# Optimization experiments

Hardware: AMD Instinct MI355X
Metric: run time of the kernel (lower is better)

The kernel has to match this reference:

```python
import jax, jax.numpy as jnp
import numpy as np

# config constants (match init_kwargs)
C = 1024
NH = 16
HS = C // NH
CHUNK = 64          # attn_chunk_size
TOPK = 32           # attn_topk
WINDOW = 4096       # kv_cache_window_size
MIN_KV = 16384      # min_kv_cache_size
MAX_KV = 32768      # max_kv_cache_size
SHORT = 4096        # short_sequence_criteria
CT = 65536          # incoming kv-cache length


def setup_inputs() -> dict:
    key = jax.random.key(0)
    ks = jax.random.split(key, 7)
    s = 1.0 / np.sqrt(C)
    return {
        "x": jax.random.normal(ks[0], (C,), jnp.float32),
        "k_cache": jax.random.normal(ks[1], (1, CT, C), jnp.float32),
        "v_cache": jax.random.normal(ks[2], (1, CT, C), jnp.float32),
        "Wr": jax.random.normal(ks[3], (C, C), jnp.float32) * s,
        "Wk": jax.random.normal(ks[4], (C, C), jnp.float32) * s,
        "Wv": jax.random.normal(ks[5], (C, C), jnp.float32) * s,
        "Wo": jax.random.normal(ks[6], (C, C), jnp.float32) * s,
    }


def _split_heads(t):  # (1, T, C) -> (1, NH, T, HS)
    return t.reshape(1, t.shape[1], NH, HS).transpose(0, 2, 1, 3)


def _update_kv_cache(q, k_cache, v_cache):
    # q: (1,1,C); caches: (1,CT,C). CT > MIN_KV so compression runs.
    past = CT - WINDOW
    kp = _split_heads(k_cache[:, :past])          # (1,NH,past,HS)
    vp = _split_heads(v_cache[:, :past])
    qh = _split_heads(q)                          # (1,NH,1,HS)
    scores = jnp.einsum("bhqd,bhkd->bhqk", qh, kp) / np.sqrt(HS)
    w = jax.nn.softmax(scores, axis=-1)           # (1,NH,1,past)
    vote = w.sum(axis=-2)                         # (1,NH,past)
    keep = MIN_KV - WINDOW                        # per-head tokens kept
    _, idx = jax.lax.top_k(vote, keep)            # (1,NH,keep), descending vote order
    kpc = jnp.take_along_axis(kp, idx[..., None], axis=2)  # (1,NH,keep,HS)
    vpc = jnp.take_along_axis(vp, idx[..., None], axis=2)
    kpc = kpc.transpose(0, 2, 1, 3).reshape(1, keep, C)
    vpc = vpc.transpose(0, 2, 1, 3).reshape(1, keep, C)
    k_new = jnp.concatenate([kpc, k_cache[:, past:]], axis=1)  # (1, MIN_KV, C)
    v_new = jnp.concatenate([vpc, v_cache[:, past:]], axis=1)
    return k_new, v_new


def reference(x, k_cache, v_cache, Wr, Wk, Wv, Wo):
    x2 = x[None, None, :]                         # (1,1,C)
    q = x2 @ Wr.T
    k = x2 @ Wk.T
    v = x2 @ Wv.T

    # CT > MAX_KV -> compress cache (eviction via attention vote per head)
    k_cache, v_cache = _update_kv_cache(q, k_cache, v_cache)
    CT2 = k_cache.shape[1]                        # MIN_KV = 16384 > SHORT -> sparse path

    num_chunks = CT2 // CHUNK
    kc = k_cache.reshape(1, num_chunks, CHUNK, C)
    vc = v_cache.reshape(1, num_chunks, CHUNK, C)
    chunk_key = kc.mean(axis=2)                   # (1,num_chunks,C)
    chunk_score = jnp.einsum("bqc,bkc->bqk", q, chunk_key)
    _, tidx = jax.lax.top_k(chunk_score[0, 0], TOPK)  # (TOPK,)
    topk_k = kc[:, tidx].reshape(1, TOPK * CHUNK, C)
    topk_v = vc[:, tidx].reshape(1, TOPK * CHUNK, C)

    k_comb = jnp.concatenate([topk_k, k], axis=1)  # (1, TOPK*CHUNK+1, C)
    v_comb = jnp.concatenate([topk_v, v], axis=1)

    qh = _split_heads(q)                          # (1,NH,1,HS)
    kh = _split_heads(k_comb)
    vh = _split_heads(v_comb)
    attn = jax.nn.softmax(
        jnp.einsum("bhqd,bhkd->bhqk", qh, kh) / np.sqrt(HS), axis=-1)
    y = jnp.einsum("bhqk,bhkd->bhqd", attn, vh)   # (1,NH,1,HS)
    y = y.transpose(0, 2, 1, 3).reshape(C)
    y = y @ Wo.T
    return y
```

## Files before the change

kernel.cpp:

```cpp
#include <hip/hip_runtime.h>
#include <stdint.h>

#define C      1024
#define NH     16
#define HS     64
#define CT     65536
#define PAST   61440
#define KEEP   12288
#define NCOMP  192
#define NSEL   32
#define NB     8192
#define NBLK   256
#define FLAGW  8

typedef unsigned long long ull;

#define LD_A(p)   __hip_atomic_load((p), __ATOMIC_RELAXED, __HIP_MEMORY_SCOPE_AGENT)
#define ST_A(p,v) __hip_atomic_store((p), (v), __ATOMIC_RELAXED, __HIP_MEMORY_SCOPE_AGENT)

__device__ __forceinline__ unsigned int desc_key(float f) {
    unsigned int b = __float_as_uint(f);
    return (b >> 31) ? b : (~b & 0x7FFFFFFFu);
}
__device__ __forceinline__ float u_to_f(unsigned int u) {
    unsigned int b = (u & 0x80000000u) ? u : (0x7FFFFFFFu - u);
    return __uint_as_float(b);
}
__device__ __forceinline__ int bin_of(float s, float hi, float scale) {
    int b = (int)((hi - s) * scale);
    return b < 0 ? 0 : (b > NB - 1 ? NB - 1 : b);
}
__device__ __forceinline__ void load_params(const unsigned* umin, const unsigned* umax,
                                            int h, float* hi, float* sc) {
    float h2 = u_to_f(umin[h]);
    float lo = u_to_f(umax[h]);
    float r = h2 - lo;
    *hi = h2;
    *sc = (r > 0.f) ? (float)(NB - 1) / r : 0.f;
}

__device__ __forceinline__ void arrive(unsigned* flag, unsigned ph) {
    __syncthreads();
    if (threadIdx.x == 0) {
        asm volatile("s_waitcnt vmcnt(0)" ::: "memory");
        ST_A(&flag[blockIdx.x * FLAGW], ph);
    }
}
__device__ __forceinline__ void wait_head(unsigned* flag, unsigned ph, int h) {
    if (threadIdx.x < 16)
        while (LD_A(&flag[(h * 16 + threadIdx.x) * FLAGW]) < ph)
            __builtin_amdgcn_s_sleep(2);
    __syncthreads();
}
__device__ __forceinline__ void wait_all(unsigned* flag, unsigned ph) {
    if (threadIdx.x < 256)
        while (LD_A(&flag[threadIdx.x * FLAGW]) < ph)
            __builtin_amdgcn_s_sleep(2);
    __syncthreads();
}

__global__ void k_proj(const float* __restrict__ x, const float* __restrict__ Wr,
                       const float* __restrict__ Wk, const float* __restrict__ Wv,
                       float* __restrict__ q, float* __restrict__ kn, float* __restrict__ vn,
                       unsigned* __restrict__ hc, unsigned* __restrict__ umin,
                       unsigned* __restrict__ umax, ull* __restrict__ cs_fix,
                       unsigned* __restrict__ flag) {
    int gid = blockIdx.x * 256 + threadIdx.x;
    for (int i = gid; i < 2 * NH * NB; i += 196608) hc[i] = 0;
    if (blockIdx.x >= 512 && blockIdx.x < 520)
        flag[(blockIdx.x - 512) * 256 + threadIdx.x] = 0u;
    if (blockIdx.x == 700) {
        if (threadIdx.x < 16) umin[threadIdx.x] = 0xFFFFFFFFu;
        else if (threadIdx.x < 32) umax[threadIdx.x - 16] = 0u;
    }
    if (blockIdx.x == 701 && threadIdx.x < 256) cs_fix[threadIdx.x] = 0ull;

    int w = blockIdx.x * (blockDim.x >> 6) + (threadIdx.x >> 6);
    int lane = threadIdx.x & 63;
    int mat = w >> 10, row = w & 1023;
    const float* W = (mat == 0) ? Wr : (mat == 1) ? Wk : Wv;
    const float4* Wrow = (const float4*)(W + (size_t)row * C);
    const float4* x4 = (const float4*)x;
    float acc = 0.f;
#pragma unroll
    for (int i = 0; i < 4; ++i) {
        float4 a = Wrow[i * 64 + lane];
        float4 b = x4[i * 64 + lane];
        acc += a.x * b.x + a.y * b.y + a.z * b.z + a.w * b.w;
    }
#pragma unroll
    for (int off = 32; off; off >>= 1) acc += __shfl_xor(acc, off);
    if (lane == 0) { (mat == 0 ? q : (mat == 1 ? kn : vn))[row] = acc; }
}

__global__ __launch_bounds__(1024, 2) void k_mega(
        const float* __restrict__ kc, const float* __restrict__ s_dummy,
        const float* __restrict__ vc,
        unsigned* __restrict__ umin, unsigned* __restrict__ umax,
        unsigned* __restrict__ hist, unsigned* __restrict__ cnt,
        ull* __restrict__ G, unsigned* __restrict__ stok,
        ull* __restrict__ cs_fix, float* __restrict__ part,
        const float* __restrict__ q, const float* __restrict__ kn,
        const float* __restrict__ vn, const float* __restrict__ Wo,
        float* __restrict__ yg, float* __restrict__ out,
        float* __restrict__ s, unsigned* __restrict__ flag) {
    const int bid = blockIdx.x, tid = threadIdx.x;
    const int lane = tid & 63, wave = tid >> 6;
    const int h = bid >> 4, seg = bid & 15;
    __shared__ __align__(16) char smem[49664];
    __shared__ unsigned shT, shN;
    __shared__ unsigned wsum[16];
    __shared__ long long wredl[16];

    {
        float (*scl)[16][17] = (float(*)[16][17])smem;
        float* smn = (float*)(smem + 18496);
        float* smx = (float*)(smem + 19520);
        const int t0 = bid * 256 + wave * 16;
        const float4* q4 = (const float4*)q;
        float4 qv[4];
#pragma unroll
        for (int i = 0; i < 4; ++i) qv[i] = q4[i * 64 + lane];
        float mnv[4] = {3.4e38f, 3.4e38f, 3.4e38f, 3.4e38f};
        float mxv[4] = {-3.4e38f, -3.4e38f, -3.4e38f, -3.4e38f};
        for (int tt = 0; tt < 16; ++tt) {
            const float4* row = (const float4*)(kc + (size_t)(t0 + tt) * C);
            float acc[4];
#pragma unroll
            for (int i = 0; i < 4; ++i) {
                float4 a = row[i * 64 + lane];
                acc[i] = a.x * qv[i].x + a.y * qv[i].y + a.z * qv[i].z + a.w * qv[i].w;
            }
#pragma unroll
            for (int off = 8; off; off >>= 1) {
#pragma unroll
                for (int i = 0; i < 4; ++i) acc[i] += __shfl_xor(acc[i], off);
            }
            if ((lane & 15) == 0) {
                int g = lane >> 4;
#pragma unroll
                for (int i = 0; i < 4; ++i) {
                    scl[wave][4 * i + g][tt] = acc[i];
                    mnv[i] = fminf(mnv[i], acc[i]);
                    mxv[i] = fmaxf(mxv[i], acc[i]);
                }
            }
        }
        __syncthreads();
        int tt2 = lane & 15;
#pragma unroll
        for (int r = 0; r < 4; ++r) {
            int h2 = r * 4 + (lane >> 4);
            ST_A(&s[(size_t)h2 * CT + t0 + tt2], scl[wave][h2][tt2]);
        }
        if (bid < 240) {
            if ((lane & 15) == 0) {
                int g = lane >> 4;
#pragma unroll
                for (int i = 0; i < 4; ++i) {
                    smn[wave * 16 + 4 * i + g] = mnv[i];
                    smx[wave * 16 + 4 * i + g] = mxv[i];
                }
            }
            __syncthreads();
            if (tid < 16) {
                float mn = smn[tid], mx = smx[tid];
                for (int w2 = 1; w2 < 16; ++w2) {
                    mn = fminf(mn, smn[w2 * 16 + tid]);
                    mx = fmaxf(mx, smx[w2 * 16 + tid]);
                }
                atomicMin(&umin[tid], desc_key(mx));
                atomicMax(&umax[tid], desc_key(mn));
            }
        } else {
            int k = tid >> 8, sub = tid & 255, hh = sub >> 4, tt = sub & 15;
            long long f = 0;
#pragma unroll
            for (int w2 = 0; w2 < 4; ++w2)
                f += llrintf(scl[4 * k + w2][hh][tt] * 16777216.f);
#pragma unroll
            for (int off = 32; off; off >>= 1) f += __shfl_xor(f, off);
            if ((tid & 63) == 0) wredl[wave] = f;
            __syncthreads();
            if ((tid & 255) == 0)
                ST_A(&cs_fix[NCOMP + (bid - 240) * 4 + k],
                     (ull)(wredl[4 * k] + wredl[4 * k + 1] + wredl[4 * k + 2] + wredl[4 * k + 3]));
        }
    }
    arrive(flag, 1); wait_all(flag, 1);

    float hi, sc; load_params(umin, umax, h, &hi, &sc);
    unsigned* lh = (unsigned*)smem;
    float* s_local = (float*)(smem + 32768);

    {
        for (int i = tid; i < NB; i += 1024) lh[i] = 0;
        __syncthreads();
        const float* sh = s + (size_t)h * CT + seg * 3840;
        for (int i = tid; i < 3840; i += 1024) {
            float v = sh[i];
            s_local[i] = v;
            atomicAdd(&lh[bin_of(v, hi, sc)], 1u);
        }
        __syncthreads();
        unsigned* gh = hist + h * NB;
        for (int i = tid; i < NB; i += 1024) {
            unsigned c = lh[i];
            if (c) atomicAdd(&gh[i], c);
        }
    }
    arrive(flag, 2); wait_head(flag, 2, h);

    {
        const unsigned* gh = hist + h * NB;
        unsigned c8[8]; unsigned loc = 0; int b0 = tid * 8;
#pragma unroll
        for (int k = 0; k < 8; ++k) { c8[k] = gh[b0 + k]; loc += c8[k]; }
        unsigned run = loc;
#pragma unroll
        for (int off = 1; off < 64; off <<= 1) {
            unsigned n = __shfl_up(run, off);
            if (lane >= off) run += n;
        }
        if (lane == 63) wsum[wave] = run;
        __syncthreads();
        if (wave == 0 && lane < 16) {
            unsigned v = wsum[lane];
#pragma unroll
            for (int off = 1; off < 16; off <<= 1) {
                unsigned n = __shfl_up(v, off);
                if (lane >= off) v += n;
            }
            wsum[lane] = v;
        }
        __syncthreads();
        unsigned r = run - loc + (wave ? wsum[wave - 1] : 0u);
#pragma unroll
        for (int k = 0; k < 8; ++k) {
            unsigned c = c8[k];
            lh[b0 + k] = r;
            unsigned inc = r + c;
            if (r < KEEP && inc >= KEEP) { shT = (unsigned)(b0 + k); shN = inc; }
            r = inc;
        }
    }
    __syncthreads();
    const unsigned T = shT, ncand = shN;

    {
        unsigned* ch = cnt + h * NB;
        ull* Gh = G + (size_t)h * 65536;
        for (int i = tid; i < 3840; i += 1024) {
            float v = s_local[i];
            int b = bin_of(v, hi, sc);
            if ((unsigned)b <= T) {
                unsigned pos = lh[b] + atomicAdd(&ch[b], 1u);
                ST_A(&Gh[pos], ((ull)desc_key(v) << 16) | (unsigned)(seg * 3840 + i));
            }
        }
    }
    arrive(flag, 3); wait_head(flag, 3, h);

    {
        ull* csl = (ull*)(smem + 48128);
        if (tid < NCOMP) csl[tid] = 0ull;
        __syncthreads();
        const ull* Gh = G + (size_t)h * 65536;
        for (unsigned p = seg * 1024 + tid; p < ncand; p += 16384) {
            ull pk = Gh[p];
            unsigned u = (unsigned)(pk >> 16);
            float v = u_to_f(u);
            int b = bin_of(v, hi, sc);
            unsigned start = lh[b];
            unsigned end = (b == NB - 1) ? ncand : lh[b + 1];
            unsigned rank = start;
            for (unsigned j = start; j < end; ++j) rank += (Gh[j] < pk) ? 1u : 0u;
            if (rank < KEEP) {
                ST_A(&stok[h * KEEP + rank], (unsigned)(pk & 0xFFFFull));
                long long f = llrintf(v * 16777216.f);
                atomicAdd(&csl[rank >> 6], (ull)f);
            }
        }
        __syncthreads();
        if (tid < NCOMP) {
            ull c = csl[tid];
            if (c) atomicAdd(&cs_fix[tid], c);
        }
    }
    arrive(flag, 4); wait_all(flag, 4);

    {
        ull* key = (ull*)smem;
        unsigned* sel_l = (unsigned*)(smem + 2048);
        float* scm = (float*)(smem + 2176);
        float* exb = (float*)(smem + 2688);
        float* vbuf = (float*)(smem + 3200);
        if (tid < 256) {
            long long v = (long long)cs_fix[tid];
            ull bb = (ull)(v + (1ll << 45));
            key[tid] = (((1ull << 46) - bb) << 8) | (unsigned)tid;
        }
        __syncthreads();
        for (unsigned k = 2; k <= 256; k <<= 1) {
            for (unsigned j = k >> 1; j > 0; j >>= 1) {
                if (tid < 256) {
                    unsigned ixj = tid ^ j;
                    if (ixj > (unsigned)tid) {
                        ull a = key[tid], b = key[ixj];
                        bool up = ((tid & k) == 0);
                        if (up ? (a > b) : (a < b)) { key[tid] = b; key[ixj] = a; }
                    }
                }
                __syncthreads();
            }
        }
        if (tid < NSEL) sel_l[tid] = (unsigned)(key[tid] & 0xFFull);
        __syncthreads();

        int su = tid >> 9, sid = tid & 511;
        int p = bid * 2 + su;
        int hh = p >> 5, ci = p & 31;
        int c = (int)sel_l[ci];
        int g = sid >> 3, q8 = sid & 7;
        int t = (c < NCOMP) ? (int)stok[hh * KEEP + c * 64 + g]
                            : (PAST + (c - NCOMP) * 64 + g);
        if (q8 == 0) scm[su * 64 + g] = s[(size_t)hh * CT + t] * 0.125f;
        __syncthreads();
        float m = -1e30f;
        for (int j = 0; j < 64; ++j) m = fmaxf(m, scm[su * 64 + j]);
        float e = expf(scm[su * 64 + g] - m);
        if (q8 == 0) exb[su * 64 + g] = e;
        const float4* vrow = (const float4*)(vc + (size_t)t * C + hh * HS);
        float4 v0 = vrow[q8 * 2], v1 = vrow[q8 * 2 + 1];
        float* vb = vbuf + su * 4352 + g * 68 + q8 * 8;
        vb[0] = e * v0.x; vb[1] = e * v0.y; vb[2] = e * v0.z; vb[3] = e * v0.w;
        vb[4] = e * v1.x; vb[5] = e * v1.y; vb[6] = e * v1.z; vb[7] = e * v1.w;
        __syncthreads();
        if (sid < 64) {
            float acc = 0.f;
            for (int g2 = 0; g2 < 64; ++g2) acc += vbuf[su * 4352 + g2 * 68 + sid];
            float* P = part + (size_t)(hh * 32 + ci) * 68;
            ST_A(&P[2 + sid], acc);
            if (sid == 0) {
                float es = 0.f;
                for (int g2 = 0; g2 < 64; ++g2) es += exb[su * 64 + g2];
                ST_A(&P[0], m);
                ST_A(&P[1], es);
            }
        }
    }
    arrive(flag, 5); wait_head(flag, 5, h);

    if (seg == 0 && tid < 64) {
        float p = q[h * 64 + tid] * kn[h * 64 + tid];
#pragma unroll
        for (int off = 32; off; off >>= 1) p += __shfl_xor(p, off);
        float a_new = p * 0.125f;
        const float* P0 = part + (size_t)h * 32 * 68;
        float m = a_new;
        for (int ci = 0; ci < 32; ++ci) m = fmaxf(m, P0[ci * 68]);
        float den = expf(a_new - m);
        float acc = den * vn[h * HS + tid];
        for (int ci = 0; ci < 32; ++ci) {
            float w = expf(P0[ci * 68] - m);
            den += w * P0[ci * 68 + 1];
            acc += w * P0[ci * 68 + 2 + tid];
        }
        ST_A(&yg[h * HS + tid], acc / den);
    }
    arrive(flag, 6); wait_all(flag, 6);

    {
        float* yl = (float*)smem;
        float* ps = (float*)(smem + 4096);
        yl[tid] = yg[tid];
        __syncthreads();
        int row = bid * 4 + (wave >> 2), qtr = wave & 3;
        const float4* Wrow = (const float4*)(Wo + (size_t)row * C) + qtr * 64;
        const float4* y4 = (const float4*)yl + qtr * 64;
        float4 a = Wrow[lane], b = y4[lane];
        float acc = a.x * b.x + a.y * b.y + a.z * b.z + a.w * b.w;
#pragma unroll
        for (int off = 32; off; off >>= 1) acc += __shfl_xor(acc, off);
        if (lane == 0) ps[wave] = acc;
        __syncthreads();
        if (tid < 4)
            out[bid * 4 + tid] = ps[tid * 4] + ps[tid * 4 + 1] + ps[tid * 4 + 2] + ps[tid * 4 + 3];
    }
}

extern "C" void kernel_launch(void* const* d_in, const int* in_sizes, int n_in,
                              void* d_out, int out_size, void* d_ws, size_t ws_size,
                              hipStream_t stream) {
    const float* x  = (const float*)d_in[0];
    const float* kc = (const float*)d_in[1];
    const float* vc = (const float*)d_in[2];
    const float* Wr = (const float*)d_in[3];
    const float* Wk = (const float*)d_in[4];
    const float* Wv = (const float*)d_in[5];
    const float* Wo = (const float*)d_in[6];
    float* out = (float*)d_out;
    char* ws = (char*)d_ws;

    float* q    = (float*)(ws + 0);
    float* kn   = (float*)(ws + 8192);
    float* vn   = (float*)(ws + 16384);
    ull* cs_fix = (ull*)(ws + 32768);
    float* yg   = (float*)(ws + 40960);
    float* part = (float*)(ws + 49152);
    unsigned* stok = (unsigned*)(ws + 196608);
    unsigned* umin = (unsigned*)(ws + 1048576);
    unsigned* umax = (unsigned*)(ws + 1048640);
    unsigned* flag = (unsigned*)(ws + 1048832);
    unsigned* hist = (unsigned*)(ws + 1114112);
    unsigned* cnt  = (unsigned*)(ws + 1638400);
    float* s = (float*)(ws + 2621440);
    ull* G = (ull*)(ws + 7340032);

    k_proj<<<768, 256, 0, stream>>>(x, Wr, Wk, Wv, q, kn, vn, hist, umin, umax, cs_fix, flag);
    k_mega<<<NBLK, 1024, 0, stream>>>(kc, s, vc, umin, umax, hist, cnt, G, stok, cs_fix,
                                      part, q, kn, vn, Wo, yg, out, s, flag);
}
```

Before: 119.2 us.

## Batch K-row loads in scoring loop, prefetch Wo, and narrow final barrier

The first-stage scoring loop now issues loads for four K-cache rows before computing, which raises memory-level parallelism per wave. The Wo row used by the output projection is now loaded before the last grid barrier, so its latency overlaps the barrier wait. That barrier becomes a targeted wait in which only the seg-0 block of each head arrives and every block polls just those 16 flags. The cost is more registers in the unrolled load loop, and the barrier now relies on the flag layout matching the head and segment mapping.

```diff
diff --git a/kernel.cpp b/kernel.cpp
--- a/kernel.cpp
+++ b/kernel.cpp
@@ -94,8 +94,7 @@
 }
 
 __global__ __launch_bounds__(1024, 2) void k_mega(
-        const float* __restrict__ kc, const float* __restrict__ s_dummy,
-        const float* __restrict__ vc,
+        const float* __restrict__ kc, const float* __restrict__ vc,
         unsigned* __restrict__ umin, unsigned* __restrict__ umax,
         unsigned* __restrict__ hist, unsigned* __restrict__ cnt,
         ull* __restrict__ G, unsigned* __restrict__ stok,
@@ -123,26 +122,34 @@
         for (int i = 0; i < 4; ++i) qv[i] = q4[i * 64 + lane];
         float mnv[4] = {3.4e38f, 3.4e38f, 3.4e38f, 3.4e38f};
         float mxv[4] = {-3.4e38f, -3.4e38f, -3.4e38f, -3.4e38f};
-        for (int tt = 0; tt < 16; ++tt) {
-            const float4* row = (const float4*)(kc + (size_t)(t0 + tt) * C);
-            float acc[4];
-#pragma unroll
-            for (int i = 0; i < 4; ++i) {
-                float4 a = row[i * 64 + lane];
-                acc[i] = a.x * qv[i].x + a.y * qv[i].y + a.z * qv[i].z + a.w * qv[i].w;
-            }
-#pragma unroll
-            for (int off = 8; off; off >>= 1) {
-#pragma unroll
-                for (int i = 0; i < 4; ++i) acc[i] += __shfl_xor(acc[i], off);
-            }
-            if ((lane & 15) == 0) {
-                int g = lane >> 4;
-#pragma unroll
-                for (int i = 0; i < 4; ++i) {
-                    scl[wave][4 * i + g][tt] = acc[i];
-                    mnv[i] = fminf(mnv[i], acc[i]);
-                    mxv[i] = fmaxf(mxv[i], acc[i]);
+        for (int tb = 0; tb < 16; tb += 4) {
+            float4 av[4][4];
+#pragma unroll
+            for (int u = 0; u < 4; ++u) {
+                const float4* row = (const float4*)(kc + (size_t)(t0 + tb + u) * C);
+#pragma unroll
+                for (int i = 0; i < 4; ++i) av[u][i] = row[i * 64 + lane];
+            }
+#pragma unroll
+            for (int u = 0; u < 4; ++u) {
+                float acc[4];
+#pragma unroll
+                for (int i = 0; i < 4; ++i)
+                    acc[i] = av[u][i].x * qv[i].x + av[u][i].y * qv[i].y
+                           + av[u][i].z * qv[i].z + av[u][i].w * qv[i].w;
+#pragma unroll
+                for (int off = 8; off; off >>= 1) {
+#pragma unroll
+                    for (int i = 0; i < 4; ++i) acc[i] += __shfl_xor(acc[i], off);
+                }
+                if ((lane & 15) == 0) {
+                    int g = lane >> 4;
+#pragma unroll
+                    for (int i = 0; i < 4; ++i) {
+                        scl[wave][4 * i + g][tb + u] = acc[i];
+                        mnv[i] = fminf(mnv[i], acc[i]);
+                        mxv[i] = fmaxf(mxv[i], acc[i]);
+                    }
                 }
             }
         }
@@ -351,6 +358,10 @@
     }
     arrive(flag, 5); wait_head(flag, 5, h);
 
+    int row = bid * 4 + (wave >> 2), qtr = wave & 3;
+    const float4* Wrow4 = (const float4*)(Wo + (size_t)row * C) + qtr * 64;
+    float4 wa = Wrow4[lane];
+
     if (seg == 0 && tid < 64) {
         float p = q[h * 64 + tid] * kn[h * 64 + tid];
 #pragma unroll
@@ -368,18 +379,19 @@
         }
         ST_A(&yg[h * HS + tid], acc / den);
     }
-    arrive(flag, 6); wait_all(flag, 6);
+    if (seg == 0) arrive(flag, 6);
+    if (tid < 16)
+        while (LD_A(&flag[(tid * 16) * FLAGW]) < 6u) __builtin_amdgcn_s_sleep(2);
+    __syncthreads();
 
     {
         float* yl = (float*)smem;
         float* ps = (float*)(smem + 4096);
         yl[tid] = yg[tid];
         __syncthreads();
-        int row = bid * 4 + (wave >> 2), qtr = wave & 3;
-        const float4* Wrow = (const float4*)(Wo + (size_t)row * C) + qtr * 64;
         const float4* y4 = (const float4*)yl + qtr * 64;
-        float4 a = Wrow[lane], b = y4[lane];
-        float acc = a.x * b.x + a.y * b.y + a.z * b.z + a.w * b.w;
+        float4 b = y4[lane];
+        float acc = wa.x * b.x + wa.y * b.y + wa.z * b.z + wa.w * b.w;
 #pragma unroll
         for (int off = 32; off; off >>= 1) acc += __shfl_xor(acc, off);
         if (lane == 0) ps[wave] = acc;
@@ -418,6 +430,6 @@
     ull* G = (ull*)(ws + 7340032);
 
     k_proj<<<768, 256, 0, stream>>>(x, Wr, Wk, Wv, q, kn, vn, hist, umin, umax, cs_fix, flag);
-    k_mega<<<NBLK, 1024, 0, stream>>>(kc, s, vc, umin, umax, hist, cnt, G, stok, cs_fix,
+    k_mega<<<NBLK, 1024, 0, stream>>>(kc, vc, umin, umax, hist, cnt, G, stok, cs_fix,
                                       part, q, kn, vn, Wo, yg, out, s, flag);
 }
```

New measurement: 117.0 us. No clear change (-1.8%).
